# Kernel optimization log

Measured on AMD Instinct MI355X. Metric: run time of the kernel, lower is better.

Reference implementation:

```python
import jax, jax.numpy as jnp
import numpy as np

DIM_DICT = 64
SIZE_DICT = 512
TEMPERATURE = 0.5
EPS_GUMBEL = 1e-10
EPS_NORM = 1e-12
EPS_PPL = 1e-7


def _l2_normalize(x, axis):
    # torch F.normalize: x / max(||x||, eps)
    n = jnp.sqrt(jnp.sum(x * x, axis=axis, keepdims=True))
    return x / jnp.maximum(n, EPS_NORM)


def setup_inputs() -> dict:
    key = jax.random.key(0)
    k1, k2, k3 = jax.random.split(key, 3)
    bs, seq_len, d = 8, 1024, 512
    z = jax.random.normal(k1, (bs, seq_len, d), dtype=jnp.float32)
    codebook = jax.random.normal(k2, (SIZE_DICT, DIM_DICT), dtype=jnp.float32)
    n_flat = bs * seq_len * (d // DIM_DICT)
    gumbel_u = jax.random.uniform(k3, (n_flat, SIZE_DICT), dtype=jnp.float32)
    kappa_q = jnp.float32(1.0)
    return {"z_from_encoder": z, "kappa_q": kappa_q, "codebook": codebook,
            "gumbel_u": gumbel_u}


def reference(z_from_encoder, kappa_q, codebook, gumbel_u):
    bs, seq_len, d = z_from_encoder.shape
    # [bs, seq, groups, dim_dict], L2-normalized along dim_dict
    z_perm = z_from_encoder.reshape(bs, seq_len, -1, DIM_DICT)
    z_norm = _l2_normalize(z_perm, axis=3)
    cb_norm = _l2_normalize(codebook, axis=1)  # [K, dim]

    # logit = -distance = kappa_q * <z, c>   -> [N, K]
    z_flat = z_norm.reshape(-1, DIM_DICT)
    logit = kappa_q * jnp.matmul(z_flat, cb_norm.T)

    log_probabilities = jax.nn.log_softmax(logit, axis=-1)
    probabilities = jnp.exp(log_probabilities)

    # gumbel-softmax sample (train path)
    g = -jnp.log(-jnp.log(gumbel_u + EPS_GUMBEL) + EPS_GUMBEL)
    encodings = jax.nn.softmax((logit + g) / TEMPERATURE, axis=-1)

    z_quantized = jnp.matmul(encodings, cb_norm).reshape(z_perm.shape)
    z_to_decoder = z_quantized.reshape(bs, seq_len, -1)

    avg_probs = jnp.mean(jax.lax.stop_gradient(probabilities), axis=0)  # [K]

    kld_discrete = jnp.sum(probabilities * log_probabilities) / bs
    kld_continuous = jnp.mean(
        jnp.sum(z_from_encoder * (z_from_encoder - z_to_decoder) * kappa_q,
                axis=(1, 2)))
    loss = kld_discrete + kld_continuous
    perplexity = jnp.exp(-jnp.sum(avg_probs * jnp.log(avg_probs + EPS_PPL)))
    return z_to_decoder, loss, perplexity
```

## Files before the change

kernel.cpp:

```cpp
#include <hip/hip_runtime.h>
#include <cstdint>
#include <cstddef>


typedef __attribute__((ext_vector_type(8))) short short8;
typedef __attribute__((ext_vector_type(4))) float f32x4;

namespace {
constexpr float kEpsG = 1e-10f;
constexpr float kEpsN = 1e-12f;
constexpr float kEpsP = 1e-7f;
constexpr float kLog2e = 1.4426950408889634f;
constexpr float kLn2 = 0.6931471805599453f;
constexpr int kSlots = 128;
constexpr int kStride = 520;
constexpr int kOffCbt = 65536;
constexpr int kOffAvg = 131072;
constexpr int kOffCS  = 133120;
constexpr int kOffAcx = 136192;
constexpr int kLdsBytes = 152576;
}

__device__ __forceinline__ float wsum64(float v) {
#pragma unroll
    for (int m = 1; m < 64; m <<= 1) v += __shfl_xor(v, m, 64);
    return v;
}
__device__ __forceinline__ uint32_t pk_bf16(float a, float b) {
    uint32_t ua = __float_as_uint(a), ub = __float_as_uint(b);
    ua += 0x7fffu + ((ua >> 16) & 1u);
    ub += 0x7fffu + ((ub >> 16) & 1u);
    return (ua >> 16) | (ub & 0xffff0000u);
}
__device__ __forceinline__ uint16_t bf16_rne(float a) {
    uint32_t ua = __float_as_uint(a);
    ua += 0x7fffu + ((ua >> 16) & 1u);
    return (uint16_t)(ua >> 16);
}
__device__ __forceinline__ float dot4(float4 v) {
    return v.x * v.x + v.y * v.y + v.z * v.z + v.w * v.w;
}

__global__ __launch_bounds__(256) void k_prep(const float* __restrict__ cb,
                                              uint16_t* __restrict__ cbN,
                                              uint16_t* __restrict__ cbNT) {
    const int row = blockIdx.x * 4 + (threadIdx.x >> 6);
    const int lane = threadIdx.x & 63;
    const float v = cb[row * 64 + lane];
    const float ss = wsum64(v * v);
    const float nv = v / fmaxf(sqrtf(ss), kEpsN);
    const uint16_t h = bf16_rne(nv);
    cbN[row * 64 + lane] = h;
    cbNT[lane * 512 + row] = h;
}

__global__ __launch_bounds__(1024, 4) void k_main(
    const float* __restrict__ z, const float* __restrict__ kqp,
    const float* __restrict__ gum, const uint16_t* __restrict__ cbN,
    const uint16_t* __restrict__ cbNT, float* __restrict__ out,
    float* __restrict__ g_part) {
    extern __shared__ float4 smem_al[];
    char* smem = (char*)smem_al;
    float* avg1 = (float*)(smem + kOffAvg);
    float (*cS)[2][16]  = (float(*)[2][16])(smem + kOffCS);
    float (*cW)[2][16]  = (float(*)[2][16])(smem + kOffCS + 1024);
    float (*cS2)[2][16] = (float(*)[2][16])(smem + kOffCS + 2048);
    float4 (*accx)[2][64] = (float4(*)[2][64])(smem + kOffAcx);

    const int tid = threadIdx.x;
    const int wv = tid >> 6;
    const int tp = wv >> 1;
    const int W = wv & 1;
    const int l = tid & 63;
    const int g = l >> 4;
    const int rh = l & 15;
    const int r0 = blockIdx.x * 128 + tp * 16;
    const int row = r0 + rh;
    const float kq = *kqp;

    if (tid < 512) avg1[tid] = 0.f;
#pragma unroll
    for (int it = 0; it < 8; ++it) {
        const int i = tid + 1024 * it;
        const uint4 v = ((const uint4*)cbN)[i];
        const int r = i >> 3, c = i & 7;
        *(uint4*)(smem + r * 128 + ((c ^ (r & 7)) << 4)) = v;
    }
#pragma unroll
    for (int it = 0; it < 4; ++it) {
        const int i = tid + 1024 * it;
        const uint4 v = ((const uint4*)cbNT)[i];
        const int d = i >> 6, c = i & 63;
        *(uint4*)(smem + kOffCbt + d * 1024 + ((c ^ (d & 7)) << 4)) = v;
    }

    const float* zr = z + (size_t)row * 64;
    const float4 a0 = *(const float4*)(zr + 8 * g);
    const float4 a1 = *(const float4*)(zr + 8 * g + 4);
    const float4 a2 = *(const float4*)(zr + 32 + 8 * g);
    const float4 a3 = *(const float4*)(zr + 36 + 8 * g);
    float ss = dot4(a0) + dot4(a1) + dot4(a2) + dot4(a3);
    ss += __shfl_xor(ss, 16, 64);
    ss += __shfl_xor(ss, 32, 64);
    const float scz = kq * kLog2e / fmaxf(sqrtf(ss), kEpsN);
    union U8 { short8 s; uint32_t u[4]; };
    U8 zb0, zb1;
    zb0.u[0] = pk_bf16(a0.x * scz, a0.y * scz);
    zb0.u[1] = pk_bf16(a0.z * scz, a0.w * scz);
    zb0.u[2] = pk_bf16(a1.x * scz, a1.y * scz);
    zb0.u[3] = pk_bf16(a1.z * scz, a1.w * scz);
    zb1.u[0] = pk_bf16(a2.x * scz, a2.y * scz);
    zb1.u[1] = pk_bf16(a2.z * scz, a2.w * scz);
    zb1.u[2] = pk_bf16(a3.x * scz, a3.y * scz);
    zb1.u[3] = pk_bf16(a3.z * scz, a3.w * scz);

    const float B1 = kq * kLog2e;
    const float* ur = gum + (size_t)row * 512 + 256 * W;

    __syncthreads();

    float S4[4] = {0.f, 0.f, 0.f, 0.f}, W4[4] = {0.f, 0.f, 0.f, 0.f};
    float S24[4] = {0.f, 0.f, 0.f, 0.f};
    f32x4 acc2[4];
#pragma unroll
    for (int dt = 0; dt < 4; ++dt) acc2[dt] = (f32x4){0.f, 0.f, 0.f, 0.f};
    const int srcA = rh + 16 * ((2 * g) & 3);
    const int srcB = rh + 16 * ((2 * g + 1) & 3);
    const bool hi = (g & 2) != 0;

#pragma unroll
    for (int T = 0; T < 4; ++T) {
        float4 u4[4];
#pragma unroll
        for (int j = 0; j < 4; ++j)
            u4[j] = *(const float4*)(ur + 64 * T + 16 * j + 4 * g);

        float pf[8];
#pragma unroll
        for (int q = 0; q < 4; ++q) {
            const int R = 256 * W + 64 * T + 16 * q + rh;
            const char* rb = smem + R * 128;
            const short8 ca0 = *(const short8*)(rb + ((g ^ (R & 7)) << 4));
            const short8 ca1 = *(const short8*)(rb + (((g + 4) ^ (R & 7)) << 4));
            f32x4 acc = {0.f, 0.f, 0.f, 0.f};
            acc = __builtin_amdgcn_mfma_f32_16x16x32_bf16(ca0, zb0.s, acc, 0, 0, 0);
            acc = __builtin_amdgcn_mfma_f32_16x16x32_bf16(ca1, zb1.s, acc, 0, 0, 0);
            const float uu[4] = {u4[q].x, u4[q].y, u4[q].z, u4[q].w};
            float e2v[4];
#pragma unroll
            for (int i = 0; i < 4; ++i) {
                const float d = acc[i] - B1;
                const float e = __builtin_amdgcn_exp2f(d);
                S4[i] += e;
                W4[i] = fmaf(d, e, W4[i]);
                const float lg = __builtin_amdgcn_logf(uu[i] + kEpsG);
                const float inr = fmaf(lg, -kLn2, kEpsG);
                const float r = __builtin_amdgcn_rcpf(inr);
                const float t = e * r;
                const float e2 = t * t;
                e2v[i] = e2;
                S24[i] += e2;
            }
            pf[2 * q] = __uint_as_float(pk_bf16(e2v[0], e2v[1]));
            pf[2 * q + 1] = __uint_as_float(pk_bf16(e2v[2], e2v[3]));
        }
#pragma unroll
        for (int ks = 0; ks < 2; ++ks) {
            const float a0lo = __shfl(pf[4 * ks + 0], srcA, 64);
            const float a1lo = __shfl(pf[4 * ks + 1], srcA, 64);
            const float a0hi = __shfl(pf[4 * ks + 2], srcA, 64);
            const float a1hi = __shfl(pf[4 * ks + 3], srcA, 64);
            const float b0lo = __shfl(pf[4 * ks + 0], srcB, 64);
            const float b1lo = __shfl(pf[4 * ks + 1], srcB, 64);
            const float b0hi = __shfl(pf[4 * ks + 2], srcB, 64);
            const float b1hi = __shfl(pf[4 * ks + 3], srcB, 64);
            U8 af;
            af.u[0] = __float_as_uint(hi ? a0hi : a0lo);
            af.u[1] = __float_as_uint(hi ? a1hi : a1lo);
            af.u[2] = __float_as_uint(hi ? b0hi : b0lo);
            af.u[3] = __float_as_uint(hi ? b1hi : b1lo);
#pragma unroll
            for (int dt = 0; dt < 4; ++dt) {
                const int D = rh + 16 * dt;
                const int c = 32 * W + 8 * T + 4 * ks + g;
                const short8 bf = *(const short8*)(smem + kOffCbt + D * 1024 +
                                                   ((c ^ (D & 7)) << 4));
                acc2[dt] = __builtin_amdgcn_mfma_f32_16x16x32_bf16(
                    af.s, bf, acc2[dt], 0, 0, 0);
            }
        }
    }

    float Sr = (S4[0] + S4[1]) + (S4[2] + S4[3]);
    float Wr = (W4[0] + W4[1]) + (W4[2] + W4[3]);
    Sr += __shfl_xor(Sr, 16, 64);
    Sr += __shfl_xor(Sr, 32, 64);
    Wr += __shfl_xor(Wr, 16, 64);
    Wr += __shfl_xor(Wr, 32, 64);
    if (g == 0) { cS[tp][W][rh] = Sr; cW[tp][W][rh] = Wr; }
    __syncthreads();
    const float St = cS[tp][0][rh] + cS[tp][1][rh];
    const float Wt = cW[tp][0][rh] + cW[tp][1][rh];
    const float inv = 1.0f / St;
    const float kldd = kLn2 * (Wt * inv - __builtin_amdgcn_logf(St));

#pragma unroll
    for (int T = 0; T < 4; ++T) {
        float ev[16];
#pragma unroll
        for (int q = 0; q < 4; ++q) {
            const int R = 256 * W + 64 * T + 16 * q + rh;
            const char* rb = smem + R * 128;
            const short8 ca0 = *(const short8*)(rb + ((g ^ (R & 7)) << 4));
            const short8 ca1 = *(const short8*)(rb + (((g + 4) ^ (R & 7)) << 4));
            f32x4 acc = {0.f, 0.f, 0.f, 0.f};
            acc = __builtin_amdgcn_mfma_f32_16x16x32_bf16(ca0, zb0.s, acc, 0, 0, 0);
            acc = __builtin_amdgcn_mfma_f32_16x16x32_bf16(ca1, zb1.s, acc, 0, 0, 0);
#pragma unroll
            for (int i = 0; i < 4; ++i)
                ev[4 * q + i] = __builtin_amdgcn_exp2f(acc[i] - B1) * inv;
        }
#pragma unroll
        for (int m = 1, nv = 8; m <= 8; m <<= 1, nv >>= 1) {
            const bool up_ = (rh & m) != 0;
#pragma unroll
            for (int t = 0; t < nv; ++t) {
                const float a = ev[t], b = ev[t + nv];
                const float keep = up_ ? b : a;
                const float send = up_ ? a : b;
                ev[t] = keep + __shfl_xor(send, m, 64);
            }
        }
        const int jr = ((rh & 1) << 3) | ((rh & 2) << 1) | ((rh & 4) >> 1) |
                       ((rh & 8) >> 3);
        atomicAdd(&avg1[256 * W + 64 * T + 16 * (jr >> 2) + 4 * g + (jr & 3)],
                  ev[0]);
    }

    float S2r = (S24[0] + S24[1]) + (S24[2] + S24[3]);
    S2r += __shfl_xor(S2r, 16, 64);
    S2r += __shfl_xor(S2r, 32, 64);
    if (g == 0) cS2[tp][W][rh] = S2r;
    if (W == 0) {
        accx[tp][0][l] = make_float4(acc2[2][0], acc2[2][1], acc2[2][2], acc2[2][3]);
        accx[tp][1][l] = make_float4(acc2[3][0], acc2[3][1], acc2[3][2], acc2[3][3]);
    }
    __syncthreads();
    const float inv2 = 1.0f / (cS2[tp][0][rh] + cS2[tp][1][rh]);
    float ivi[4];
#pragma unroll
    for (int i = 0; i < 4; ++i) ivi[i] = __shfl(inv2, 4 * g + i, 64);
    float4 x0, x1;
    if (W == 1) { x0 = accx[tp][0][l]; x1 = accx[tp][1][l]; }
    __syncthreads();
    if (W == 1) {
        accx[tp][0][l] = make_float4(acc2[0][0], acc2[0][1], acc2[0][2], acc2[0][3]);
        accx[tp][1][l] = make_float4(acc2[1][0], acc2[1][1], acc2[1][2], acc2[1][3]);
    }
    __syncthreads();
    if (W == 0) { x0 = accx[tp][0][l]; x1 = accx[tp][1][l]; }

    float kldc = 0.f;
#define EPI(OV, XV, DT)                                                       \
    {                                                                         \
        const float oq[4] = {OV[0] + XV.x, OV[1] + XV.y, OV[2] + XV.z,        \
                             OV[3] + XV.w};                                   \
        _Pragma("unroll") for (int i = 0; i < 4; ++i) {                       \
            const float q = oq[i] * ivi[i];                                   \
            const size_t oi = (size_t)(r0 + 4 * g + i) * 64 + rh + 16 * (DT); \
            out[oi] = q;                                                      \
            const float zv = z[oi];                                           \
            kldc = fmaf(zv, zv - q, kldc);                                    \
        }                                                                     \
    }
    if (W == 0) {
        EPI(acc2[0], x0, 0)
        EPI(acc2[1], x1, 1)
    } else {
        EPI(acc2[2], x0, 2)
        EPI(acc2[3], x1, 3)
    }

    const int slot = blockIdx.x & (kSlots - 1);
    float* gp = g_part + (size_t)slot * kStride;
    const float kc = wsum64(kldc) * kq;
    const float kd = wsum64(kldd) * 0.25f;
    if (l == 0) {
        atomicAdd(&gp[513], kc);
        if (W == 0) atomicAdd(&gp[512], kd);
    }
    __syncthreads();
    if (tid < 512) atomicAdd(&gp[tid], avg1[tid]);
}

__global__ __launch_bounds__(512) void k_final(const float* __restrict__ g_part,
                                               float* __restrict__ out) {
    __shared__ float red[8];
    const int tid = threadIdx.x;
    float sacc = 0.f;
#pragma unroll 8
    for (int i = 0; i < kSlots; ++i) sacc += g_part[(size_t)i * kStride + tid];
    const float avg = sacc * (1.0f / 65536.0f);
    const float t = avg * __logf(avg + kEpsP);
    const float sw = wsum64(t);
    if ((tid & 63) == 0) red[tid >> 6] = sw;
    __syncthreads();
    if (tid == 0) {
        float tot = 0.f;
#pragma unroll
        for (int i = 0; i < 8; ++i) tot += red[i];
        float sc0 = 0.f, sc1 = 0.f;
        for (int i = 0; i < kSlots; ++i) {
            sc0 += g_part[(size_t)i * kStride + 512];
            sc1 += g_part[(size_t)i * kStride + 513];
        }
        out[4194304] = (sc0 + sc1) * 0.125f;
        out[4194305] = __expf(-tot);
    }
}

extern "C" void kernel_launch(void* const* d_in, const int* in_sizes, int n_in,
                              void* d_out, int out_size, void* d_ws, size_t ws_size,
                              hipStream_t stream) {
    (void)in_sizes; (void)n_in; (void)out_size; (void)ws_size;
    const float* z   = (const float*)d_in[0];
    const float* kq  = (const float*)d_in[1];
    const float* cb  = (const float*)d_in[2];
    const float* gum = (const float*)d_in[3];
    float* out = (float*)d_out;

    uint16_t* cbN  = (uint16_t*)d_ws;
    uint16_t* cbNT = cbN + 32768;
    float* g_part  = (float*)(cbNT + 32768);

    (void)hipFuncSetAttribute((const void*)k_main,
                              hipFuncAttributeMaxDynamicSharedMemorySize,
                              kLdsBytes);
    (void)hipMemsetAsync(g_part, 0, kSlots * kStride * sizeof(float), stream);
    k_prep<<<128, 256, 0, stream>>>(cb, cbN, cbNT);
    k_main<<<512, 1024, kLdsBytes, stream>>>(z, kq, gum, cbN, cbNT, out, g_part);
    k_final<<<1, 512, 0, stream>>>(g_part, out);
}
```

Measured before the change: 85.79 us.

## Split each row tile across four waves and cache first-pass exponentials

Each 16-row tile is now shared by four waves instead of two, each covering 128 codebook entries. Blocks shrink to 64 rows, so the grid doubles to 1024 blocks. The first-pass exp values are kept in registers as packed bf16, so the second pass no longer reruns the logit MFMAs and exp2. Cross-wave partial sums of the quantized output are combined with LDS atomics, and the gumbel loads are issued before the barrier. In exchange, every block still copies the full 128 KB codebook into LDS, so total codebook staging traffic doubles, and the avg-prob term now uses bf16-rounded exponentials.

```diff
diff --git a/kernel.cpp b/kernel.cpp
--- a/kernel.cpp
+++ b/kernel.cpp
@@ -17,7 +17,7 @@
 constexpr int kOffCbt = 65536;
 constexpr int kOffAvg = 131072;
 constexpr int kOffCS  = 133120;
-constexpr int kOffAcx = 136192;
+constexpr int kOffAcz = 136192;
 constexpr int kLdsBytes = 152576;
 }
 
@@ -54,7 +54,7 @@
     cbNT[lane * 512 + row] = h;
 }
 
-__global__ __launch_bounds__(1024, 4) void k_main(
+__global__ __launch_bounds__(1024) void k_main(
     const float* __restrict__ z, const float* __restrict__ kqp,
     const float* __restrict__ gum, const uint16_t* __restrict__ cbN,
     const uint16_t* __restrict__ cbNT, float* __restrict__ out,
@@ -62,23 +62,25 @@
     extern __shared__ float4 smem_al[];
     char* smem = (char*)smem_al;
     float* avg1 = (float*)(smem + kOffAvg);
-    float (*cS)[2][16]  = (float(*)[2][16])(smem + kOffCS);
-    float (*cW)[2][16]  = (float(*)[2][16])(smem + kOffCS + 1024);
-    float (*cS2)[2][16] = (float(*)[2][16])(smem + kOffCS + 2048);
-    float4 (*accx)[2][64] = (float4(*)[2][64])(smem + kOffAcx);
+    float (*cS)[4][16]  = (float(*)[4][16])(smem + kOffCS);
+    float (*cW)[4][16]  = (float(*)[4][16])(smem + kOffCS + 1024);
+    float (*cS2)[4][16] = (float(*)[4][16])(smem + kOffCS + 2048);
+    float* accZ = (float*)(smem + kOffAcz);
 
     const int tid = threadIdx.x;
     const int wv = tid >> 6;
-    const int tp = wv >> 1;
-    const int W = wv & 1;
+    const int tp = wv >> 2;
+    const int W = wv & 3;
     const int l = tid & 63;
     const int g = l >> 4;
     const int rh = l & 15;
-    const int r0 = blockIdx.x * 128 + tp * 16;
+    const int r0 = blockIdx.x * 64 + tp * 16;
     const int row = r0 + rh;
     const float kq = *kqp;
 
     if (tid < 512) avg1[tid] = 0.f;
+#pragma unroll
+    for (int j = 0; j < 4; ++j) accZ[tid + 1024 * j] = 0.f;
 #pragma unroll
     for (int it = 0; it < 8; ++it) {
         const int i = tid + 1024 * it;
@@ -115,10 +117,18 @@
     zb1.u[3] = pk_bf16(a3.z * scz, a3.w * scz);
 
     const float B1 = kq * kLog2e;
-    const float* ur = gum + (size_t)row * 512 + 256 * W;
+
+    const float* ur = gum + (size_t)row * 512 + 128 * W;
+    float4 u0[4], u1[4];
+#pragma unroll
+    for (int j = 0; j < 4; ++j) u0[j] = *(const float4*)(ur + 16 * j + 4 * g);
+#pragma unroll
+    for (int j = 0; j < 4; ++j)
+        u1[j] = *(const float4*)(ur + 64 + 16 * j + 4 * g);
 
     __syncthreads();
 
+    uint32_t epk[16];
     float S4[4] = {0.f, 0.f, 0.f, 0.f}, W4[4] = {0.f, 0.f, 0.f, 0.f};
     float S24[4] = {0.f, 0.f, 0.f, 0.f};
     f32x4 acc2[4];
@@ -129,28 +139,25 @@
     const bool hi = (g & 2) != 0;
 
 #pragma unroll
-    for (int T = 0; T < 4; ++T) {
-        float4 u4[4];
-#pragma unroll
-        for (int j = 0; j < 4; ++j)
-            u4[j] = *(const float4*)(ur + 64 * T + 16 * j + 4 * g);
-
+    for (int T = 0; T < 2; ++T) {
         float pf[8];
 #pragma unroll
         for (int q = 0; q < 4; ++q) {
-            const int R = 256 * W + 64 * T + 16 * q + rh;
+            const int R = 128 * W + 64 * T + 16 * q + rh;
             const char* rb = smem + R * 128;
             const short8 ca0 = *(const short8*)(rb + ((g ^ (R & 7)) << 4));
             const short8 ca1 = *(const short8*)(rb + (((g + 4) ^ (R & 7)) << 4));
             f32x4 acc = {0.f, 0.f, 0.f, 0.f};
             acc = __builtin_amdgcn_mfma_f32_16x16x32_bf16(ca0, zb0.s, acc, 0, 0, 0);
             acc = __builtin_amdgcn_mfma_f32_16x16x32_bf16(ca1, zb1.s, acc, 0, 0, 0);
-            const float uu[4] = {u4[q].x, u4[q].y, u4[q].z, u4[q].w};
-            float e2v[4];
+            const float4 uq = (T == 0) ? u0[q] : u1[q];
+            const float uu[4] = {uq.x, uq.y, uq.z, uq.w};
+            float e4[4], e2v[4];
 #pragma unroll
             for (int i = 0; i < 4; ++i) {
                 const float d = acc[i] - B1;
                 const float e = __builtin_amdgcn_exp2f(d);
+                e4[i] = e;
                 S4[i] += e;
                 W4[i] = fmaf(d, e, W4[i]);
                 const float lg = __builtin_amdgcn_logf(uu[i] + kEpsG);
@@ -161,6 +168,8 @@
                 e2v[i] = e2;
                 S24[i] += e2;
             }
+            epk[8 * T + 2 * q] = pk_bf16(e4[0], e4[1]);
+            epk[8 * T + 2 * q + 1] = pk_bf16(e4[2], e4[3]);
             pf[2 * q] = __uint_as_float(pk_bf16(e2v[0], e2v[1]));
             pf[2 * q + 1] = __uint_as_float(pk_bf16(e2v[2], e2v[3]));
         }
@@ -182,7 +191,7 @@
 #pragma unroll
             for (int dt = 0; dt < 4; ++dt) {
                 const int D = rh + 16 * dt;
-                const int c = 32 * W + 8 * T + 4 * ks + g;
+                const int c = 16 * W + 8 * T + 4 * ks + g;
                 const short8 bf = *(const short8*)(smem + kOffCbt + D * 1024 +
                                                    ((c ^ (D & 7)) << 4));
                 acc2[dt] = __builtin_amdgcn_mfma_f32_16x16x32_bf16(
@@ -199,27 +208,24 @@
     Wr += __shfl_xor(Wr, 32, 64);
     if (g == 0) { cS[tp][W][rh] = Sr; cW[tp][W][rh] = Wr; }
     __syncthreads();
-    const float St = cS[tp][0][rh] + cS[tp][1][rh];
-    const float Wt = cW[tp][0][rh] + cW[tp][1][rh];
+    const float St = (cS[tp][0][rh] + cS[tp][1][rh]) +
+                     (cS[tp][2][rh] + cS[tp][3][rh]);
+    const float Wt = (cW[tp][0][rh] + cW[tp][1][rh]) +
+                     (cW[tp][2][rh] + cW[tp][3][rh]);
     const float inv = 1.0f / St;
     const float kldd = kLn2 * (Wt * inv - __builtin_amdgcn_logf(St));
 
 #pragma unroll
-    for (int T = 0; T < 4; ++T) {
+    for (int T = 0; T < 2; ++T) {
         float ev[16];
 #pragma unroll
-        for (int q = 0; q < 4; ++q) {
-            const int R = 256 * W + 64 * T + 16 * q + rh;
-            const char* rb = smem + R * 128;
-            const short8 ca0 = *(const short8*)(rb + ((g ^ (R & 7)) << 4));
-            const short8 ca1 = *(const short8*)(rb + (((g + 4) ^ (R & 7)) << 4));
-            f32x4 acc = {0.f, 0.f, 0.f, 0.f};
-            acc = __builtin_amdgcn_mfma_f32_16x16x32_bf16(ca0, zb0.s, acc, 0, 0, 0);
-            acc = __builtin_amdgcn_mfma_f32_16x16x32_bf16(ca1, zb1.s, acc, 0, 0, 0);
-#pragma unroll
-            for (int i = 0; i < 4; ++i)
-                ev[4 * q + i] = __builtin_amdgcn_exp2f(acc[i] - B1) * inv;
-        }
+        for (int k2 = 0; k2 < 8; ++k2) {
+            const uint32_t pe = epk[8 * T + k2];
+            ev[2 * k2] = __uint_as_float(pe << 16);
+            ev[2 * k2 + 1] = __uint_as_float(pe & 0xffff0000u);
+        }
+#pragma unroll
+        for (int j = 0; j < 16; ++j) ev[j] *= inv;
 #pragma unroll
         for (int m = 1, nv = 8; m <= 8; m <<= 1, nv >>= 1) {
             const bool up_ = (rh & m) != 0;
@@ -233,7 +239,7 @@
         }
         const int jr = ((rh & 1) << 3) | ((rh & 2) << 1) | ((rh & 4) >> 1) |
                        ((rh & 8) >> 3);
-        atomicAdd(&avg1[256 * W + 64 * T + 16 * (jr >> 2) + 4 * g + (jr & 3)],
+        atomicAdd(&avg1[128 * W + 64 * T + 16 * (jr >> 2) + 4 * g + (jr & 3)],
                   ev[0]);
     }
 
@@ -241,55 +247,47 @@
     S2r += __shfl_xor(S2r, 16, 64);
     S2r += __shfl_xor(S2r, 32, 64);
     if (g == 0) cS2[tp][W][rh] = S2r;
-    if (W == 0) {
-        accx[tp][0][l] = make_float4(acc2[2][0], acc2[2][1], acc2[2][2], acc2[2][3]);
-        accx[tp][1][l] = make_float4(acc2[3][0], acc2[3][1], acc2[3][2], acc2[3][3]);
+#pragma unroll
+    for (int dt = 0; dt < 4; ++dt) {
+        if (dt == W) continue;
+        float* dst = accZ + ((tp * 4 + dt) * 64 + l) * 4;
+        atomicAdd(dst + 0, acc2[dt][0]);
+        atomicAdd(dst + 1, acc2[dt][1]);
+        atomicAdd(dst + 2, acc2[dt][2]);
+        atomicAdd(dst + 3, acc2[dt][3]);
     }
     __syncthreads();
-    const float inv2 = 1.0f / (cS2[tp][0][rh] + cS2[tp][1][rh]);
+
+    const float inv2 = 1.0f / ((cS2[tp][0][rh] + cS2[tp][1][rh]) +
+                               (cS2[tp][2][rh] + cS2[tp][3][rh]));
     float ivi[4];
 #pragma unroll
     for (int i = 0; i < 4; ++i) ivi[i] = __shfl(inv2, 4 * g + i, 64);
-    float4 x0, x1;
-    if (W == 1) { x0 = accx[tp][0][l]; x1 = accx[tp][1][l]; }
-    __syncthreads();
-    if (W == 1) {
-        accx[tp][0][l] = make_float4(acc2[0][0], acc2[0][1], acc2[0][2], acc2[0][3]);
-        accx[tp][1][l] = make_float4(acc2[1][0], acc2[1][1], acc2[1][2], acc2[1][3]);
-    }
-    __syncthreads();
-    if (W == 0) { x0 = accx[tp][0][l]; x1 = accx[tp][1][l]; }
+
+    const f32x4 own = (W == 0) ? acc2[0] : (W == 1) ? acc2[1]
+                     : (W == 2) ? acc2[2] : acc2[3];
+    const float4 az = *(const float4*)(accZ + ((tp * 4 + W) * 64 + l) * 4);
 
     float kldc = 0.f;
-#define EPI(OV, XV, DT)                                                       \
-    {                                                                         \
-        const float oq[4] = {OV[0] + XV.x, OV[1] + XV.y, OV[2] + XV.z,        \
-                             OV[3] + XV.w};                                   \
-        _Pragma("unroll") for (int i = 0; i < 4; ++i) {                       \
-            const float q = oq[i] * ivi[i];                                   \
-            const size_t oi = (size_t)(r0 + 4 * g + i) * 64 + rh + 16 * (DT); \
-            out[oi] = q;                                                      \
-            const float zv = z[oi];                                           \
-            kldc = fmaf(zv, zv - q, kldc);                                    \
-        }                                                                     \
-    }
-    if (W == 0) {
-        EPI(acc2[0], x0, 0)
-        EPI(acc2[1], x1, 1)
-    } else {
-        EPI(acc2[2], x0, 2)
-        EPI(acc2[3], x1, 3)
-    }
-
+#pragma unroll
+    for (int i = 0; i < 4; ++i) {
+        const float pq = (i == 0) ? (own[0] + az.x) : (i == 1) ? (own[1] + az.y)
+                        : (i == 2) ? (own[2] + az.z) : (own[3] + az.w);
+        const float qv = pq * ivi[i];
+        const size_t oi = (size_t)(r0 + 4 * g + i) * 64 + rh + 16 * W;
+        out[oi] = qv;
+        const float zv = z[oi];
+        kldc = fmaf(zv, zv - qv, kldc);
+    }
+
+    const float kc = wsum64(kldc) * kq;
+    const float kd = wsum64(kldd) * 0.25f;
     const int slot = blockIdx.x & (kSlots - 1);
     float* gp = g_part + (size_t)slot * kStride;
-    const float kc = wsum64(kldc) * kq;
-    const float kd = wsum64(kldd) * 0.25f;
     if (l == 0) {
         atomicAdd(&gp[513], kc);
         if (W == 0) atomicAdd(&gp[512], kd);
     }
-    __syncthreads();
     if (tid < 512) atomicAdd(&gp[tid], avg1[tid]);
 }
 
@@ -338,6 +336,6 @@
                               kLdsBytes);
     (void)hipMemsetAsync(g_part, 0, kSlots * kStride * sizeof(float), stream);
     k_prep<<<128, 256, 0, stream>>>(cb, cbN, cbNT);
-    k_main<<<512, 1024, kLdsBytes, stream>>>(z, kq, gum, cbN, cbNT, out, g_part);
+    k_main<<<1024, 1024, kLdsBytes, stream>>>(z, kq, gum, cbN, cbNT, out, g_part);
     k_final<<<1, 512, 0, stream>>>(g_part, out);
 }
```

Result: slower. 172.9 us (+101.6%).
